# Performance work log

Measured on AMD Instinct MI355X. Metric: run time of the kernel, lower is better.

## Reference

```python
import jax, jax.numpy as jnp
import numpy as np

B, L, D, H = 2, 1024, 1024, 16
HD = D // H  # 64


def _skew(x):
    # x: (BH, L, 2L-1) -> (BH, L, L); Music-Transformer skew trick.
    BH, Lx, _ = x.shape
    x = jnp.pad(x, ((0, 0), (0, 0), (1, 0)))            # (BH, L, 2L)
    x = x.reshape(BH, 2 * Lx * Lx)                        # flatten
    x = jnp.pad(x, ((0, 0), (0, Lx - 1)))                 # append L-1 zeros
    x = x.reshape(BH, Lx + 1, 2 * Lx - 1)
    return x[:, :Lx, Lx - 1:]


def setup_inputs() -> dict:
    key = jax.random.key(0)
    ks = jax.random.split(key, 10)
    s = 1.0 / np.sqrt(D)
    return {
        "x": jax.random.normal(ks[0], (B, L, D), jnp.float32),
        "Wq": jax.random.normal(ks[1], (D, D), jnp.float32) * s,
        "bq": jnp.zeros((D,), jnp.float32),
        "Wk": jax.random.normal(ks[2], (D, D), jnp.float32) * s,
        "bk": jnp.zeros((D,), jnp.float32),
        "Wv": jax.random.normal(ks[3], (D, D), jnp.float32) * s,
        "bv": jnp.zeros((D,), jnp.float32),
        "Wo": jax.random.normal(ks[4], (D, D), jnp.float32) * s,
        "bo": jnp.zeros((D,), jnp.float32),
        "rel_pos_emb": jax.random.normal(ks[5], (2 * L - 1, HD), jnp.float32),
    }


def reference(x, Wq, bq, Wk, bk, Wv, bv, Wo, bo, rel_pos_emb):
    Bx, Lx, Dx = x.shape
    hd = Dx // H
    scale = hd ** (-0.5)
    # projections (torch Linear: x @ W.T + b)
    q = (x @ Wq.T + bq).reshape(Bx, Lx, H, hd).transpose(0, 2, 1, 3)  # (B,H,L,hd)
    k = (x @ Wk.T + bk).reshape(Bx, Lx, H, hd).transpose(0, 2, 1, 3)
    v = (x @ Wv.T + bv).reshape(Bx, Lx, H, hd).transpose(0, 2, 1, 3)
    scores = jnp.einsum('bhid,bhjd->bhij', q, k)                      # (B,H,L,L)
    rel = jnp.einsum('bhid,rd->bhir', q, rel_pos_emb)                 # (B,H,L,2L-1)
    rel = _skew(rel.reshape(Bx * H, Lx, 2 * Lx - 1)).reshape(Bx, H, Lx, Lx)
    attn = jax.nn.softmax((scores + rel) * scale, axis=-1)
    ctx = jnp.einsum('bhij,bhjd->bhid', attn, v)                      # (B,H,L,hd)
    ctx = ctx.transpose(0, 2, 1, 3).reshape(Bx, Lx, Dx)
    return ctx @ Wo.T + bo
```

## Files before the change

kernel.cpp:

```cpp
#include <hip/hip_runtime.h>
#include <hip/hip_bf16.h>

typedef __bf16 bf16_t;
typedef __bf16 bf16x8 __attribute__((ext_vector_type(8)));
typedef __bf16 bf16x4 __attribute__((ext_vector_type(4)));
typedef float f32x4 __attribute__((ext_vector_type(4)));

#define B_ 2
#define L_ 1024
#define D_ 1024
#define H_ 16
#define HD_ 64

static __device__ __forceinline__ bf16x8 cvt8(const float4 a, const float4 b) {
    bf16x8 o;
    o[0] = (bf16_t)a.x; o[1] = (bf16_t)a.y;
    o[2] = (bf16_t)a.z; o[3] = (bf16_t)a.w;
    o[4] = (bf16_t)b.x; o[5] = (bf16_t)b.y;
    o[6] = (bf16_t)b.z; o[7] = (bf16_t)b.w;
    return o;
}

__global__ __launch_bounds__(256) void prep_kernel(
    const float* __restrict__ x, const float* __restrict__ E,
    bf16_t* __restrict__ xb, bf16_t* __restrict__ Eb) {
    const int bid = blockIdx.x;
    if (bid < 2048) {
        const int i = bid * 256 + threadIdx.x;
        const float4 v = ((const float4*)x)[i];
        bf16x4 o;
        o[0] = (bf16_t)v.x; o[1] = (bf16_t)v.y;
        o[2] = (bf16_t)v.z; o[3] = (bf16_t)v.w;
        ((bf16x4*)xb)[i] = o;
    } else {
        const int idx = (bid - 2048) * 256 + threadIdx.x;
        if (idx < 64) Eb[idx] = (bf16_t)0.f;
        if (idx < 2047 * 64) Eb[64 + idx] = (bf16_t)E[idx];
    }
}

__global__ __launch_bounds__(256) void qkv_gemm_kernel(
    const bf16_t* __restrict__ xb,
    const float* __restrict__ Wqf, const float* __restrict__ Wkf,
    const float* __restrict__ Wvf,
    const float* __restrict__ bq, const float* __restrict__ bk2,
    const float* __restrict__ bv2,
    bf16_t* __restrict__ qbh, bf16_t* __restrict__ kbh,
    bf16_t* __restrict__ vtb) {
    constexpr int K = D_;
    __shared__ __align__(16) bf16_t As[64][72];
    __shared__ __align__(16) bf16_t Bs[64][72];

    const int z = blockIdx.z;
    const float* Wf = (z == 0) ? Wqf : (z == 1) ? Wkf : Wvf;
    const float* bias = (z == 0) ? bq : (z == 1) ? bk2 : bv2;
    const float alpha = (z == 0) ? 0.18033688011112043f : 1.0f;

    const int tid = threadIdx.x;
    const int m0 = blockIdx.y * 64;
    const int n0 = blockIdx.x * 64;
    const int wave = tid >> 6;
    const int lane = tid & 63;
    const int wm = (wave >> 1) << 5;
    const int wn = (wave & 1) << 5;
    const int lrow = lane & 15;
    const int quad = lane >> 4;
    const int r0 = tid >> 3;
    const int c8 = (tid & 7) << 3;

    f32x4 acc[2][2] = {};

    uint4 pA0 = *(const uint4*)&xb[(size_t)(m0 + r0) * K + c8];
    uint4 pA1 = *(const uint4*)&xb[(size_t)(m0 + r0 + 32) * K + c8];
    float4 pB0a = *(const float4*)&Wf[(size_t)(n0 + r0) * K + c8];
    float4 pB0b = *(const float4*)&Wf[(size_t)(n0 + r0) * K + c8 + 4];
    float4 pB1a = *(const float4*)&Wf[(size_t)(n0 + r0 + 32) * K + c8];
    float4 pB1b = *(const float4*)&Wf[(size_t)(n0 + r0 + 32) * K + c8 + 4];

    for (int k0 = 0; k0 < K; k0 += 64) {
        *(uint4*)&As[r0][c8] = pA0;
        *(uint4*)&As[r0 + 32][c8] = pA1;
        *(bf16x8*)&Bs[r0][c8] = cvt8(pB0a, pB0b);
        *(bf16x8*)&Bs[r0 + 32][c8] = cvt8(pB1a, pB1b);
        const int kn = (k0 + 64 < K) ? k0 + 64 : k0;
        pA0 = *(const uint4*)&xb[(size_t)(m0 + r0) * K + kn + c8];
        pA1 = *(const uint4*)&xb[(size_t)(m0 + r0 + 32) * K + kn + c8];
        pB0a = *(const float4*)&Wf[(size_t)(n0 + r0) * K + kn + c8];
        pB0b = *(const float4*)&Wf[(size_t)(n0 + r0) * K + kn + c8 + 4];
        pB1a = *(const float4*)&Wf[(size_t)(n0 + r0 + 32) * K + kn + c8];
        pB1b = *(const float4*)&Wf[(size_t)(n0 + r0 + 32) * K + kn + c8 + 4];
        __syncthreads();

#pragma unroll
        for (int kc = 0; kc < 2; ++kc) {
            bf16x8 af[2], bfr[2];
            af[0]  = *(const bf16x8*)&As[wm + lrow][kc * 32 + 8 * quad];
            af[1]  = *(const bf16x8*)&As[wm + 16 + lrow][kc * 32 + 8 * quad];
            bfr[0] = *(const bf16x8*)&Bs[wn + lrow][kc * 32 + 8 * quad];
            bfr[1] = *(const bf16x8*)&Bs[wn + 16 + lrow][kc * 32 + 8 * quad];
#pragma unroll
            for (int t = 0; t < 2; ++t)
#pragma unroll
                for (int u = 0; u < 2; ++u)
                    acc[t][u] = __builtin_amdgcn_mfma_f32_16x16x32_bf16(
                        af[t], bfr[u], acc[t][u], 0, 0, 0);
        }
        __syncthreads();
    }

#pragma unroll
    for (int t = 0; t < 2; ++t) {
#pragma unroll
        for (int u = 0; u < 2; ++u) {
            const int col = n0 + wn + u * 16 + lrow;
            const float bvv = bias[col];
            const int h = col >> 6, d = col & 63;
            if (z < 2) {
                bf16_t* outp = z ? kbh : qbh;
#pragma unroll
                for (int r = 0; r < 4; ++r) {
                    const int row = m0 + wm + t * 16 + quad * 4 + r;
                    const int b = row >> 10, i = row & 1023;
                    outp[((size_t)((b * H_ + h) * L_ + i)) * HD_ + d] =
                        (bf16_t)((acc[t][u][r] + bvv) * alpha);
                }
            } else {
                const int row0 = m0 + wm + t * 16 + quad * 4;
                const int b = row0 >> 10, i = row0 & 1023;
                bf16x4 pk;
#pragma unroll
                for (int r = 0; r < 4; ++r) pk[r] = (bf16_t)(acc[t][u][r] + bvv);
                *(bf16x4*)&vtb[((size_t)((b * H_ + h) * HD_ + d)) * L_ + i] = pk;
            }
        }
    }
}

__global__ __launch_bounds__(256) void out_gemm_kernel(
    const bf16_t* __restrict__ A, const float* __restrict__ Wf,
    const float* __restrict__ bias, float* __restrict__ outF) {
    constexpr int K = D_;
    __shared__ __align__(16) bf16_t As[64][72];
    __shared__ __align__(16) bf16_t Bs[64][72];

    const int tid = threadIdx.x;
    const int m0 = blockIdx.y * 64;
    const int n0 = blockIdx.x * 64;
    const int wave = tid >> 6;
    const int lane = tid & 63;
    const int wm = (wave >> 1) << 5;
    const int wn = (wave & 1) << 5;
    const int lrow = lane & 15;
    const int quad = lane >> 4;
    const int r0 = tid >> 3;
    const int c8 = (tid & 7) << 3;

    f32x4 acc[2][2] = {};

    uint4 pA0 = *(const uint4*)&A[(size_t)(m0 + r0) * K + c8];
    uint4 pA1 = *(const uint4*)&A[(size_t)(m0 + r0 + 32) * K + c8];
    float4 pB0a = *(const float4*)&Wf[(size_t)(n0 + r0) * K + c8];
    float4 pB0b = *(const float4*)&Wf[(size_t)(n0 + r0) * K + c8 + 4];
    float4 pB1a = *(const float4*)&Wf[(size_t)(n0 + r0 + 32) * K + c8];
    float4 pB1b = *(const float4*)&Wf[(size_t)(n0 + r0 + 32) * K + c8 + 4];

    for (int k0 = 0; k0 < K; k0 += 64) {
        *(uint4*)&As[r0][c8] = pA0;
        *(uint4*)&As[r0 + 32][c8] = pA1;
        *(bf16x8*)&Bs[r0][c8] = cvt8(pB0a, pB0b);
        *(bf16x8*)&Bs[r0 + 32][c8] = cvt8(pB1a, pB1b);
        const int kn = (k0 + 64 < K) ? k0 + 64 : k0;
        pA0 = *(const uint4*)&A[(size_t)(m0 + r0) * K + kn + c8];
        pA1 = *(const uint4*)&A[(size_t)(m0 + r0 + 32) * K + kn + c8];
        pB0a = *(const float4*)&Wf[(size_t)(n0 + r0) * K + kn + c8];
        pB0b = *(const float4*)&Wf[(size_t)(n0 + r0) * K + kn + c8 + 4];
        pB1a = *(const float4*)&Wf[(size_t)(n0 + r0 + 32) * K + kn + c8];
        pB1b = *(const float4*)&Wf[(size_t)(n0 + r0 + 32) * K + kn + c8 + 4];
        __syncthreads();

#pragma unroll
        for (int kc = 0; kc < 2; ++kc) {
            bf16x8 af[2], bfr[2];
            af[0]  = *(const bf16x8*)&As[wm + lrow][kc * 32 + 8 * quad];
            af[1]  = *(const bf16x8*)&As[wm + 16 + lrow][kc * 32 + 8 * quad];
            bfr[0] = *(const bf16x8*)&Bs[wn + lrow][kc * 32 + 8 * quad];
            bfr[1] = *(const bf16x8*)&Bs[wn + 16 + lrow][kc * 32 + 8 * quad];
#pragma unroll
            for (int t = 0; t < 2; ++t)
#pragma unroll
                for (int u = 0; u < 2; ++u)
                    acc[t][u] = __builtin_amdgcn_mfma_f32_16x16x32_bf16(
                        af[t], bfr[u], acc[t][u], 0, 0, 0);
        }
        __syncthreads();
    }

#pragma unroll
    for (int t = 0; t < 2; ++t) {
#pragma unroll
        for (int u = 0; u < 2; ++u) {
            const int col = n0 + wn + u * 16 + lrow;
            const float bvv = bias[col];
#pragma unroll
            for (int r = 0; r < 4; ++r) {
                const int row = m0 + wm + t * 16 + quad * 4 + r;
                outF[(size_t)row * D_ + col] = acc[t][u][r] + bvv;
            }
        }
    }
}

__global__ __launch_bounds__(256) void fattn_kernel(
    const bf16_t* __restrict__ qbh, const bf16_t* __restrict__ kbh,
    const bf16_t* __restrict__ vtb, const bf16_t* __restrict__ Eb,
    bf16_t* __restrict__ ctx) {
    __shared__ __align__(16) char smem[33792];
    float (*Om)[32][64] = (float(*)[32][64])smem;
    float (*ml)[32]     = (float(*)[32])(smem + 32768);

    const int tid = threadIdx.x;
    const int w = tid >> 6;
    const int lane = tid & 63;
    const int q4 = lane >> 4;
    const int n = lane & 15;
    const int bh = blockIdx.y;
    const int b = bh >> 4;
    const int h = bh & 15;
    const int ib = blockIdx.x * 32;

    bf16_t* band = (bf16_t*)smem + (size_t)w * (96 * 44);
    bf16_t* ps = band;

    bf16x8 ones;
#pragma unroll
    for (int e = 0; e < 8; ++e) ones[e] = (bf16_t)1.0f;

    bf16x8 aq[2][2];
#pragma unroll
    for (int m = 0; m < 2; ++m) {
        const bf16x8* qrow =
            (const bf16x8*)(qbh + ((size_t)bh * L_ + ib + 16 * m + n) * HD_);
        aq[m][0] = qrow[q4];
        aq[m][1] = qrow[4 + q4];
    }

    const bf16_t* vbase = vtb + (size_t)bh * HD_ * L_;

    f32x4 o[2][4] = {};
    float l_r[2][4] = {};

    for (int t = 0; t < 4; ++t) {
        const int j0 = w * 256 + t * 64;

        bf16x8 bk[4][2];
#pragma unroll
        for (int u = 0; u < 4; ++u)
#pragma unroll
            for (int kc = 0; kc < 2; ++kc)
                bk[u][kc] = *(const bf16x8*)(kbh +
                    ((size_t)bh * L_ + j0 + 16 * u + n) * HD_ + kc * 32 + 8 * q4);

        const int rbase = j0 - ib + 992;
#pragma unroll
        for (int up = 0; up < 6; ++up) {
            f32x4 rc[2] = {};
#pragma unroll
            for (int kc = 0; kc < 2; ++kc) {
                const bf16x8 be = *(const bf16x8*)(Eb +
                    ((size_t)(rbase + 16 * up + n)) * HD_ + kc * 32 + 8 * q4);
#pragma unroll
                for (int m = 0; m < 2; ++m)
                    rc[m] = __builtin_amdgcn_mfma_f32_16x16x32_bf16(
                        aq[m][kc], be, rc[m], 0, 0, 0);
            }
#pragma unroll
            for (int m = 0; m < 2; ++m) {
                bf16x4 pk;
#pragma unroll
                for (int r = 0; r < 4; ++r) pk[r] = (bf16_t)rc[m][r];
                *(bf16x4*)&band[(size_t)(16 * up + n) * 44 + 16 * m + 4 * q4] = pk;
            }
        }

        f32x4 s[2][4] = {};
#pragma unroll
        for (int u = 0; u < 4; ++u)
#pragma unroll
            for (int kc = 0; kc < 2; ++kc)
#pragma unroll
                for (int m = 0; m < 2; ++m)
                    s[m][u] = __builtin_amdgcn_mfma_f32_16x16x32_bf16(
                        aq[m][kc], bk[u][kc], s[m][u], 0, 0, 0);

        bf16x8 vf[4][2];
#pragma unroll
        for (int u = 0; u < 4; ++u)
#pragma unroll
            for (int kc = 0; kc < 2; ++kc)
                vf[u][kc] = *(const bf16x8*)(vbase +
                    ((size_t)(16 * u + n)) * L_ + j0 + kc * 32 + 8 * q4);

#pragma unroll
        for (int m = 0; m < 2; ++m)
#pragma unroll
            for (int u = 0; u < 4; ++u)
#pragma unroll
                for (int r = 0; r < 4; ++r) {
                    const int row = 16 * m + 4 * q4 + r;
                    const float sv = s[m][u][r] +
                        (float)band[(size_t)(16 * u + n - row + 31) * 44 + row];
                    s[m][u][r] = __builtin_amdgcn_exp2f(sv - 24.0f);
                }

#pragma unroll
        for (int m = 0; m < 2; ++m)
#pragma unroll
            for (int u = 0; u < 4; ++u)
#pragma unroll
                for (int r = 0; r < 4; ++r)
                    ps[(size_t)(16 * m + 4 * q4 + r) * 72 + 16 * u + n] =
                        (bf16_t)s[m][u][r];

        bf16x8 pa[2][2];
#pragma unroll
        for (int m = 0; m < 2; ++m) {
            pa[m][0] = *(const bf16x8*)&ps[(size_t)(16 * m + n) * 72 + 8 * q4];
            pa[m][1] = *(const bf16x8*)&ps[(size_t)(16 * m + n) * 72 + 32 + 8 * q4];
        }

#pragma unroll
        for (int m = 0; m < 2; ++m) {
            f32x4 z = {};
            z = __builtin_amdgcn_mfma_f32_16x16x32_bf16(pa[m][0], ones, z, 0, 0, 0);
            z = __builtin_amdgcn_mfma_f32_16x16x32_bf16(pa[m][1], ones, z, 0, 0, 0);
#pragma unroll
            for (int r = 0; r < 4; ++r)
                l_r[m][r] += z[r];
        }

        __builtin_amdgcn_s_setprio(1);
#pragma unroll
        for (int u = 0; u < 4; ++u)
#pragma unroll
            for (int kc = 0; kc < 2; ++kc)
#pragma unroll
                for (int m = 0; m < 2; ++m)
                    o[m][u] = __builtin_amdgcn_mfma_f32_16x16x32_bf16(
                        pa[m][kc], vf[u][kc], o[m][u], 0, 0, 0);
        __builtin_amdgcn_s_setprio(0);
    }

    __syncthreads();
#pragma unroll
    for (int m = 0; m < 2; ++m)
#pragma unroll
        for (int u = 0; u < 4; ++u)
#pragma unroll
            for (int r = 0; r < 4; ++r)
                Om[w][16 * m + 4 * q4 + r][16 * u + n] = o[m][u][r];
    if (n == 0) {
#pragma unroll
        for (int m = 0; m < 2; ++m)
#pragma unroll
            for (int r = 0; r < 4; ++r)
                ml[w][16 * m + 4 * q4 + r] = l_r[m][r];
    }
    __syncthreads();

    {
        const int row = tid >> 3;
        const int c0 = (tid & 7) * 8;
        const float inv = 1.f / (ml[0][row] + ml[1][row] +
                                 ml[2][row] + ml[3][row]);
        bf16_t* dst = ctx + ((size_t)(b * L_ + ib + row)) * D_ + h * HD_ + c0;
#pragma unroll
        for (int cc = 0; cc < 8; ++cc) {
            const int col = c0 + cc;
            const float val = (Om[0][row][col] + Om[1][row][col] +
                               Om[2][row][col] + Om[3][row][col]) * inv;
            dst[cc] = (bf16_t)val;
        }
    }
}

extern "C" void kernel_launch(void* const* d_in, const int* in_sizes, int n_in,
                              void* d_out, int out_size, void* d_ws,
                              size_t ws_size, hipStream_t stream) {
    const float* x   = (const float*)d_in[0];
    const float* Wq  = (const float*)d_in[1];
    const float* bq  = (const float*)d_in[2];
    const float* Wk  = (const float*)d_in[3];
    const float* bk  = (const float*)d_in[4];
    const float* Wv  = (const float*)d_in[5];
    const float* bv  = (const float*)d_in[6];
    const float* Wo  = (const float*)d_in[7];
    const float* bo  = (const float*)d_in[8];
    const float* E   = (const float*)d_in[9];
    float* out = (float*)d_out;

    char* ws = (char*)d_ws;
    const size_t MB = 1024u * 1024u;
    bf16_t* xb   = (bf16_t*)(ws);
    bf16_t* qbh  = (bf16_t*)(ws + 4 * MB);
    bf16_t* kbh  = (bf16_t*)(ws + 8 * MB);
    bf16_t* vtb  = (bf16_t*)(ws + 12 * MB);
    bf16_t* ctxb = (bf16_t*)(ws + 16 * MB);
    bf16_t* Eb   = (bf16_t*)(ws + 20 * MB);

    prep_kernel<<<2560, 256, 0, stream>>>(x, E, xb, Eb);

    dim3 gq(D_ / 64, (B_ * L_) / 64, 3);
    qkv_gemm_kernel<<<gq, 256, 0, stream>>>(xb, Wq, Wk, Wv, bq, bk, bv,
                                            qbh, kbh, vtb);

    dim3 ga(L_ / 32, B_ * H_);
    fattn_kernel<<<ga, 256, 0, stream>>>(qbh, kbh, vtb, Eb, ctxb);

    dim3 gg(D_ / 64, (B_ * L_) / 64);
    out_gemm_kernel<<<gg, 256, 0, stream>>>(ctxb, Wo, bo, out);
}
```

Measured before the change: 180.6 us.

## Use single-wave 64x64 tiles in projection GEMMs and drop block barriers

Both the QKV and output projection GEMMs now launch one 64-lane wave per 64x64 tile instead of four waves. That single wave stages all rows of A and B, computes a 4x4 grid of 16x16 MFMA tiles and handles the full epilogue. Because only one wave touches the shared-memory tiles, the __syncthreads barriers are removed, which also removes barrier stalls and gives more MFMA work per LDS fragment load. The cost is higher register pressure (64 accumulators plus 8-deep prefetch buffers) and four times fewer waves per CU to hide global-memory latency. Correctness also now depends on the single wave's in-order LDS behaviour rather than explicit barriers.

```diff
diff --git a/kernel.cpp b/kernel.cpp
--- a/kernel.cpp
+++ b/kernel.cpp
@@ -39,7 +39,7 @@
     }
 }
 
-__global__ __launch_bounds__(256) void qkv_gemm_kernel(
+__global__ __launch_bounds__(64) void qkv_gemm_kernel(
     const bf16_t* __restrict__ xb,
     const float* __restrict__ Wqf, const float* __restrict__ Wkf,
     const float* __restrict__ Wvf,
@@ -56,76 +56,78 @@
     const float* bias = (z == 0) ? bq : (z == 1) ? bk2 : bv2;
     const float alpha = (z == 0) ? 0.18033688011112043f : 1.0f;
 
-    const int tid = threadIdx.x;
+    const int lane = threadIdx.x;
+    const int n = lane & 15;
+    const int q4 = lane >> 4;
+    const int srow = lane >> 3;
+    const int sc8 = (lane & 7) << 3;
     const int m0 = blockIdx.y * 64;
     const int n0 = blockIdx.x * 64;
-    const int wave = tid >> 6;
-    const int lane = tid & 63;
-    const int wm = (wave >> 1) << 5;
-    const int wn = (wave & 1) << 5;
-    const int lrow = lane & 15;
-    const int quad = lane >> 4;
-    const int r0 = tid >> 3;
-    const int c8 = (tid & 7) << 3;
-
-    f32x4 acc[2][2] = {};
-
-    uint4 pA0 = *(const uint4*)&xb[(size_t)(m0 + r0) * K + c8];
-    uint4 pA1 = *(const uint4*)&xb[(size_t)(m0 + r0 + 32) * K + c8];
-    float4 pB0a = *(const float4*)&Wf[(size_t)(n0 + r0) * K + c8];
-    float4 pB0b = *(const float4*)&Wf[(size_t)(n0 + r0) * K + c8 + 4];
-    float4 pB1a = *(const float4*)&Wf[(size_t)(n0 + r0 + 32) * K + c8];
-    float4 pB1b = *(const float4*)&Wf[(size_t)(n0 + r0 + 32) * K + c8 + 4];
+
+    f32x4 acc[4][4] = {};
+
+    uint4 pA[8];
+    float4 pBa[8], pBb[8];
+#pragma unroll
+    for (int i = 0; i < 8; ++i) {
+        const int row = i * 8 + srow;
+        pA[i]  = *(const uint4*)&xb[(size_t)(m0 + row) * K + sc8];
+        pBa[i] = *(const float4*)&Wf[(size_t)(n0 + row) * K + sc8];
+        pBb[i] = *(const float4*)&Wf[(size_t)(n0 + row) * K + sc8 + 4];
+    }
 
     for (int k0 = 0; k0 < K; k0 += 64) {
-        *(uint4*)&As[r0][c8] = pA0;
-        *(uint4*)&As[r0 + 32][c8] = pA1;
-        *(bf16x8*)&Bs[r0][c8] = cvt8(pB0a, pB0b);
-        *(bf16x8*)&Bs[r0 + 32][c8] = cvt8(pB1a, pB1b);
+#pragma unroll
+        for (int i = 0; i < 8; ++i) {
+            const int row = i * 8 + srow;
+            *(uint4*)&As[row][sc8] = pA[i];
+            *(bf16x8*)&Bs[row][sc8] = cvt8(pBa[i], pBb[i]);
+        }
         const int kn = (k0 + 64 < K) ? k0 + 64 : k0;
-        pA0 = *(const uint4*)&xb[(size_t)(m0 + r0) * K + kn + c8];
-        pA1 = *(const uint4*)&xb[(size_t)(m0 + r0 + 32) * K + kn + c8];
-        pB0a = *(const float4*)&Wf[(size_t)(n0 + r0) * K + kn + c8];
-        pB0b = *(const float4*)&Wf[(size_t)(n0 + r0) * K + kn + c8 + 4];
-        pB1a = *(const float4*)&Wf[(size_t)(n0 + r0 + 32) * K + kn + c8];
-        pB1b = *(const float4*)&Wf[(size_t)(n0 + r0 + 32) * K + kn + c8 + 4];
-        __syncthreads();
+#pragma unroll
+        for (int i = 0; i < 8; ++i) {
+            const int row = i * 8 + srow;
+            pA[i]  = *(const uint4*)&xb[(size_t)(m0 + row) * K + kn + sc8];
+            pBa[i] = *(const float4*)&Wf[(size_t)(n0 + row) * K + kn + sc8];
+            pBb[i] = *(const float4*)&Wf[(size_t)(n0 + row) * K + kn + sc8 + 4];
+        }
 
 #pragma unroll
         for (int kc = 0; kc < 2; ++kc) {
-            bf16x8 af[2], bfr[2];
-            af[0]  = *(const bf16x8*)&As[wm + lrow][kc * 32 + 8 * quad];
-            af[1]  = *(const bf16x8*)&As[wm + 16 + lrow][kc * 32 + 8 * quad];
-            bfr[0] = *(const bf16x8*)&Bs[wn + lrow][kc * 32 + 8 * quad];
-            bfr[1] = *(const bf16x8*)&Bs[wn + 16 + lrow][kc * 32 + 8 * quad];
-#pragma unroll
-            for (int t = 0; t < 2; ++t)
-#pragma unroll
-                for (int u = 0; u < 2; ++u)
+            bf16x8 af[4], bfr[4];
+#pragma unroll
+            for (int t = 0; t < 4; ++t)
+                af[t] = *(const bf16x8*)&As[16 * t + n][kc * 32 + 8 * q4];
+#pragma unroll
+            for (int u = 0; u < 4; ++u)
+                bfr[u] = *(const bf16x8*)&Bs[16 * u + n][kc * 32 + 8 * q4];
+#pragma unroll
+            for (int t = 0; t < 4; ++t)
+#pragma unroll
+                for (int u = 0; u < 4; ++u)
                     acc[t][u] = __builtin_amdgcn_mfma_f32_16x16x32_bf16(
                         af[t], bfr[u], acc[t][u], 0, 0, 0);
         }
-        __syncthreads();
-    }
-
-#pragma unroll
-    for (int t = 0; t < 2; ++t) {
-#pragma unroll
-        for (int u = 0; u < 2; ++u) {
-            const int col = n0 + wn + u * 16 + lrow;
+    }
+
+#pragma unroll
+    for (int t = 0; t < 4; ++t) {
+#pragma unroll
+        for (int u = 0; u < 4; ++u) {
+            const int col = n0 + u * 16 + n;
             const float bvv = bias[col];
             const int h = col >> 6, d = col & 63;
             if (z < 2) {
                 bf16_t* outp = z ? kbh : qbh;
 #pragma unroll
                 for (int r = 0; r < 4; ++r) {
-                    const int row = m0 + wm + t * 16 + quad * 4 + r;
+                    const int row = m0 + t * 16 + q4 * 4 + r;
                     const int b = row >> 10, i = row & 1023;
                     outp[((size_t)((b * H_ + h) * L_ + i)) * HD_ + d] =
                         (bf16_t)((acc[t][u][r] + bvv) * alpha);
                 }
             } else {
-                const int row0 = m0 + wm + t * 16 + quad * 4;
+                const int row0 = m0 + t * 16 + q4 * 4;
                 const int b = row0 >> 10, i = row0 & 1023;
                 bf16x4 pk;
 #pragma unroll
@@ -136,74 +138,76 @@
     }
 }
 
-__global__ __launch_bounds__(256) void out_gemm_kernel(
+__global__ __launch_bounds__(64) void out_gemm_kernel(
     const bf16_t* __restrict__ A, const float* __restrict__ Wf,
     const float* __restrict__ bias, float* __restrict__ outF) {
     constexpr int K = D_;
     __shared__ __align__(16) bf16_t As[64][72];
     __shared__ __align__(16) bf16_t Bs[64][72];
 
-    const int tid = threadIdx.x;
+    const int lane = threadIdx.x;
+    const int n = lane & 15;
+    const int q4 = lane >> 4;
+    const int srow = lane >> 3;
+    const int sc8 = (lane & 7) << 3;
     const int m0 = blockIdx.y * 64;
     const int n0 = blockIdx.x * 64;
-    const int wave = tid >> 6;
-    const int lane = tid & 63;
-    const int wm = (wave >> 1) << 5;
-    const int wn = (wave & 1) << 5;
-    const int lrow = lane & 15;
-    const int quad = lane >> 4;
-    const int r0 = tid >> 3;
-    const int c8 = (tid & 7) << 3;
-
-    f32x4 acc[2][2] = {};
-
-    uint4 pA0 = *(const uint4*)&A[(size_t)(m0 + r0) * K + c8];
-    uint4 pA1 = *(const uint4*)&A[(size_t)(m0 + r0 + 32) * K + c8];
-    float4 pB0a = *(const float4*)&Wf[(size_t)(n0 + r0) * K + c8];
-    float4 pB0b = *(const float4*)&Wf[(size_t)(n0 + r0) * K + c8 + 4];
-    float4 pB1a = *(const float4*)&Wf[(size_t)(n0 + r0 + 32) * K + c8];
-    float4 pB1b = *(const float4*)&Wf[(size_t)(n0 + r0 + 32) * K + c8 + 4];
+
+    f32x4 acc[4][4] = {};
+
+    uint4 pA[8];
+    float4 pBa[8], pBb[8];
+#pragma unroll
+    for (int i = 0; i < 8; ++i) {
+        const int row = i * 8 + srow;
+        pA[i]  = *(const uint4*)&A[(size_t)(m0 + row) * K + sc8];
+        pBa[i] = *(const float4*)&Wf[(size_t)(n0 + row) * K + sc8];
+        pBb[i] = *(const float4*)&Wf[(size_t)(n0 + row) * K + sc8 + 4];
+    }
 
     for (int k0 = 0; k0 < K; k0 += 64) {
-        *(uint4*)&As[r0][c8] = pA0;
-        *(uint4*)&As[r0 + 32][c8] = pA1;
-        *(bf16x8*)&Bs[r0][c8] = cvt8(pB0a, pB0b);
-        *(bf16x8*)&Bs[r0 + 32][c8] = cvt8(pB1a, pB1b);
+#pragma unroll
+        for (int i = 0; i < 8; ++i) {
+            const int row = i * 8 + srow;
+            *(uint4*)&As[row][sc8] = pA[i];
+            *(bf16x8*)&Bs[row][sc8] = cvt8(pBa[i], pBb[i]);
+        }
         const int kn = (k0 + 64 < K) ? k0 + 64 : k0;
-        pA0 = *(const uint4*)&A[(size_t)(m0 + r0) * K + kn + c8];
-        pA1 = *(const uint4*)&A[(size_t)(m0 + r0 + 32) * K + kn + c8];
-        pB0a = *(const float4*)&Wf[(size_t)(n0 + r0) * K + kn + c8];
-        pB0b = *(const float4*)&Wf[(size_t)(n0 + r0) * K + kn + c8 + 4];
-        pB1a = *(const float4*)&Wf[(size_t)(n0 + r0 + 32) * K + kn + c8];
-        pB1b = *(const float4*)&Wf[(size_t)(n0 + r0 + 32) * K + kn + c8 + 4];
-        __syncthreads();
+#pragma unroll
+        for (int i = 0; i < 8; ++i) {
+            const int row = i * 8 + srow;
+            pA[i]  = *(const uint4*)&A[(size_t)(m0 + row) * K + kn + sc8];
+            pBa[i] = *(const float4*)&Wf[(size_t)(n0 + row) * K + kn + sc8];
+            pBb[i] = *(const float4*)&Wf[(size_t)(n0 + row) * K + kn + sc8 + 4];
+        }
 
 #pragma unroll
         for (int kc = 0; kc < 2; ++kc) {
-            bf16x8 af[2], bfr[2];
-            af[0]  = *(const bf16x8*)&As[wm + lrow][kc * 32 + 8 * quad];
-            af[1]  = *(const bf16x8*)&As[wm + 16 + lrow][kc * 32 + 8 * quad];
-            bfr[0] = *(const bf16x8*)&Bs[wn + lrow][kc * 32 + 8 * quad];
-            bfr[1] = *(const bf16x8*)&Bs[wn + 16 + lrow][kc * 32 + 8 * quad];
-#pragma unroll
-            for (int t = 0; t < 2; ++t)
-#pragma unroll
-                for (int u = 0; u < 2; ++u)
+            bf16x8 af[4], bfr[4];
+#pragma unroll
+            for (int t = 0; t < 4; ++t)
+                af[t] = *(const bf16x8*)&As[16 * t + n][kc * 32 + 8 * q4];
+#pragma unroll
+            for (int u = 0; u < 4; ++u)
+                bfr[u] = *(const bf16x8*)&Bs[16 * u + n][kc * 32 + 8 * q4];
+#pragma unroll
+            for (int t = 0; t < 4; ++t)
+#pragma unroll
+                for (int u = 0; u < 4; ++u)
                     acc[t][u] = __builtin_amdgcn_mfma_f32_16x16x32_bf16(
                         af[t], bfr[u], acc[t][u], 0, 0, 0);
         }
-        __syncthreads();
-    }
-
-#pragma unroll
-    for (int t = 0; t < 2; ++t) {
-#pragma unroll
-        for (int u = 0; u < 2; ++u) {
-            const int col = n0 + wn + u * 16 + lrow;
+    }
+
+#pragma unroll
+    for (int t = 0; t < 4; ++t) {
+#pragma unroll
+        for (int u = 0; u < 4; ++u) {
+            const int col = n0 + u * 16 + n;
             const float bvv = bias[col];
 #pragma unroll
             for (int r = 0; r < 4; ++r) {
-                const int row = m0 + wm + t * 16 + quad * 4 + r;
+                const int row = m0 + t * 16 + q4 * 4 + r;
                 outF[(size_t)row * D_ + col] = acc[t][u][r] + bvv;
             }
         }
@@ -410,12 +414,12 @@
     prep_kernel<<<2560, 256, 0, stream>>>(x, E, xb, Eb);
 
     dim3 gq(D_ / 64, (B_ * L_) / 64, 3);
-    qkv_gemm_kernel<<<gq, 256, 0, stream>>>(xb, Wq, Wk, Wv, bq, bk, bv,
-                                            qbh, kbh, vtb);
+    qkv_gemm_kernel<<<gq, 64, 0, stream>>>(xb, Wq, Wk, Wv, bq, bk, bv,
+                                           qbh, kbh, vtb);
 
     dim3 ga(L_ / 32, B_ * H_);
     fattn_kernel<<<ga, 256, 0, stream>>>(qbh, kbh, vtb, Eb, ctxb);
 
     dim3 gg(D_ / 64, (B_ * L_) / 64);
-    out_gemm_kernel<<<gg, 256, 0, stream>>>(ctxb, Wo, bo, out);
-}
+    out_gemm_kernel<<<gg, 64, 0, stream>>>(ctxb, Wo, bo, out);
+}
```

Result: slower. 236.1 us (+30.7%).
